# Kernel optimization log

Hardware: AMD Instinct MI355X
Metric: run time of the kernel (lower is better)

The kernel has to match this reference:

```python
import jax, jax.numpy as jnp
import numpy as np

B, TY, TX, TT, H, VS, VT = 32, 64, 64, 64, 512, 32000, 32000


def setup_inputs() -> dict:
    key = jax.random.key(0)
    ks = jax.random.split(key, 12)
    s = 0.05  # weight scale for numerical sanity
    return {
        "y_hidden": jax.random.normal(ks[0], (B, TY, H), jnp.float32),
        "y_hidden_null": jax.random.normal(ks[1], (1, H), jnp.float32),
        "target_state": jax.random.normal(ks[2], (B, TT, H), jnp.float32),
        "W_em": jax.random.normal(ks[3], (H, H), jnp.float32) * s,
        "b_em": jnp.zeros((H,), jnp.float32),
        "W_sv": jax.random.normal(ks[4], (H, VS), jnp.float32) * s,
        "b_sv": jnp.zeros((VS,), jnp.float32),
        "W_tv": jax.random.normal(ks[5], (H, VT), jnp.float32) * s,
        "b_tv": jnp.zeros((VT,), jnp.float32),
        "sources": jax.random.randint(ks[6], (B, TX), 0, VS, jnp.int32),
        "targets": jax.random.randint(ks[7], (B, TT), 0, VT, jnp.int32),
        "target_lengths": jax.random.randint(ks[8], (B,), 1, TT + 1, jnp.int32),
    }


def reference(y_hidden, y_hidden_null, target_state, W_em, b_em, W_sv, b_sv,
              W_tv, b_tv, sources, targets, target_lengths):
    # ---- emission (get_emission) ----
    ts = jnp.tanh(y_hidden @ W_em + b_em)            # (B, Ty, H)
    tsn = jnp.tanh(y_hidden_null @ W_em + b_em)      # (1, H)
    em_sm = jax.nn.softmax(ts @ W_sv + b_sv, axis=-1)        # (B, Ty, Vs)
    null_sm = jax.nn.softmax(tsn @ W_sv + b_sv, axis=-1)     # (1, Vs)
    # vectorized replacement of tf.map_fn + tf.gather: per-batch gather of source token columns
    em_g = jnp.take_along_axis(em_sm, sources[:, None, :], axis=-1)  # (B, Ty, Tx)
    null_g = null_sm[0][sources]                                     # (B, Tx)
    null_tiled = jnp.broadcast_to(null_g[:, None, :], (sources.shape[0], ts.shape[1], sources.shape[1]))
    emission_prob = jnp.concatenate([em_g, null_tiled], axis=1)      # (B, 2*Ty, Tx)

    # ---- reconstruction (get_target); keep_prob = 1 so dropout is identity ----
    tgt_sm = jax.nn.softmax(target_state @ W_tv + b_tv, axis=-1)     # (B, Tt, Vt)
    target_predicted = jnp.argmax(tgt_sm, axis=-1)                   # (B, Tt)
    # gather[t, targets[t]] then * eye then reduce_sum == diagonal pick: prob of own token
    target_prob = jnp.take_along_axis(tgt_sm, targets[:, :, None].astype(jnp.int32), axis=-1)[..., 0]  # (B, Tt)
    Tt = targets.shape[1]
    target_mask = (jnp.arange(Tt)[None, :] < target_lengths[:, None]).astype(target_prob.dtype)
    reconstruction_expectation = target_prob * target_mask
    reconstruction_expectation_log = jnp.log(target_prob) * target_mask
    return emission_prob, reconstruction_expectation, reconstruction_expectation_log, target_predicted
```

## Files before the change

### kernel.cpp

```cpp
#include <hip/hip_runtime.h>
#include <math.h>

#define H 512
#define V 32000
#define NVB 250

typedef unsigned short ushort_t;
typedef __attribute__((ext_vector_type(8))) short short8;
typedef __attribute__((ext_vector_type(4))) float f32x4;

__device__ __forceinline__ unsigned short f2bf(float x) {
    unsigned int u; __builtin_memcpy(&u, &x, 4);
    unsigned int r = (u + 0x7fffu + ((u >> 16) & 1u)) >> 16;
    return (unsigned short)r;
}
__device__ __forceinline__ float bfu2f(unsigned short h) {
    unsigned int u = ((unsigned int)h) << 16;
    float f; __builtin_memcpy(&f, &u, 4);
    return f;
}

__device__ __forceinline__ void t2_insert(float& m1, int& c1, float& m2, int& c2,
                                          float v, int idx) {
    if (v > m1 || (v == m1 && idx < c1)) { m2 = m1; c2 = c1; m1 = v; c1 = idx; }
    else if (v > m2 || (v == m2 && idx < c2)) { m2 = v; c2 = idx; }
}

__global__ __launch_bounds__(256) void k_emstate(
    const float* __restrict__ y_hidden, const float* __restrict__ y_null,
    const float* __restrict__ W, const float* __restrict__ bias,
    float* __restrict__ ts)
{
    const int NR = 2049;
    __shared__ float As[16][64];
    __shared__ float Bs[16][64];
    int rb = blockIdx.y, cb = blockIdx.x;
    int row0 = rb * 64, col0 = cb * 64;
    int tid = threadIdx.x;
    int tr = tid >> 4, tc = tid & 15;
    float acc[4][4] = {};
    for (int k0 = 0; k0 < H; k0 += 16) {
        {
            int r = tid >> 2;
            int kk = (tid & 3) << 2;
            int row = row0 + r;
            float4 v = make_float4(0.f, 0.f, 0.f, 0.f);
            if (row < 2048)       v = *(const float4*)&y_hidden[row * H + k0 + kk];
            else if (row == 2048) v = *(const float4*)&y_null[k0 + kk];
            As[kk + 0][r] = v.x; As[kk + 1][r] = v.y;
            As[kk + 2][r] = v.z; As[kk + 3][r] = v.w;
            int bk = tid >> 4, bc = (tid & 15) << 2;
            *(float4*)&Bs[bk][bc] = *(const float4*)&W[(k0 + bk) * H + col0 + bc];
        }
        __syncthreads();
#pragma unroll
        for (int kk = 0; kk < 16; ++kk) {
            float4 a = *(float4*)&As[kk][tr * 4];
            float4 b = *(float4*)&Bs[kk][tc * 4];
            float av[4] = {a.x, a.y, a.z, a.w};
            float bv[4] = {b.x, b.y, b.z, b.w};
#pragma unroll
            for (int i = 0; i < 4; i++)
#pragma unroll
                for (int j = 0; j < 4; j++) acc[i][j] += av[i] * bv[j];
        }
        __syncthreads();
    }
#pragma unroll
    for (int i = 0; i < 4; i++) {
        int row = row0 + tr * 4 + i;
        if (row >= NR) break;
#pragma unroll
        for (int j = 0; j < 4; j++) {
            int col = col0 + tc * 4 + j;
            ts[(size_t)row * H + col] = tanhf(acc[i][j] + bias[col]);
        }
    }
}

__global__ __launch_bounds__(256) void k_packA(
    const float* __restrict__ A, int nvalid, int nb16,
    ushort_t* __restrict__ Ph, ushort_t* __restrict__ Pl)
{
    int c = blockIdx.x * 256 + threadIdx.x;
    if (c >= nb16 * 1024) return;
    int n16 = c >> 10, rem = c & 1023, k32 = rem >> 6, l = rem & 63;
    int m = n16 * 16 + (l & 15);
    int k = k32 * 32 + (l >> 4) * 8;
    float v[8];
    if (m < nvalid) {
        *(float4*)&v[0] = *(const float4*)&A[(size_t)m * H + k];
        *(float4*)&v[4] = *(const float4*)&A[(size_t)m * H + k + 4];
    } else {
#pragma unroll
        for (int j = 0; j < 8; ++j) v[j] = 0.f;
    }
    unsigned int hh[4], lo[4];
#pragma unroll
    for (int p = 0; p < 4; ++p) {
        unsigned short h0 = f2bf(v[2 * p]), h1 = f2bf(v[2 * p + 1]);
        hh[p] = (unsigned int)h0 | ((unsigned int)h1 << 16);
        unsigned short l0 = f2bf(v[2 * p] - bfu2f(h0));
        unsigned short l1 = f2bf(v[2 * p + 1] - bfu2f(h1));
        lo[p] = (unsigned int)l0 | ((unsigned int)l1 << 16);
    }
    size_t o = ((size_t)n16 * 16 + k32) * 512 + l * 8;
    *(uint4*)&Ph[o] = make_uint4(hh[0], hh[1], hh[2], hh[3]);
    *(uint4*)&Pl[o] = make_uint4(lo[0], lo[1], lo[2], lo[3]);
}

__global__ __launch_bounds__(256) void k_packW(
    const float* __restrict__ W,
    ushort_t* __restrict__ Ph, ushort_t* __restrict__ Pl)
{
    int c = blockIdx.x * 256 + threadIdx.x;
    int n16 = c >> 10, rem = c & 1023, k32 = rem >> 6, l = rem & 63;
    int n = n16 * 16 + (l & 15);
    int k = k32 * 32 + (l >> 4) * 8;
    float v[8];
#pragma unroll
    for (int j = 0; j < 8; ++j) v[j] = W[(size_t)(k + j) * V + n];
    unsigned int hh[4], lo[4];
#pragma unroll
    for (int p = 0; p < 4; ++p) {
        unsigned short h0 = f2bf(v[2 * p]), h1 = f2bf(v[2 * p + 1]);
        hh[p] = (unsigned int)h0 | ((unsigned int)h1 << 16);
        unsigned short l0 = f2bf(v[2 * p] - bfu2f(h0));
        unsigned short l1 = f2bf(v[2 * p + 1] - bfu2f(h1));
        lo[p] = (unsigned int)l0 | ((unsigned int)l1 << 16);
    }
    size_t o = ((size_t)n16 * 16 + k32) * 512 + l * 8;
    *(uint4*)&Ph[o] = make_uint4(hh[0], hh[1], hh[2], hh[3]);
    *(uint4*)&Pl[o] = make_uint4(lo[0], lo[1], lo[2], lo[3]);
}

template<bool TOP2>
__global__ __launch_bounds__(256, 2) void k_gemm(
    int nrb,
    const ushort_t* __restrict__ Ah, const ushort_t* __restrict__ Al,
    const ushort_t* __restrict__ Bh, const ushort_t* __restrict__ Bl,
    const float* __restrict__ bias,
    float* __restrict__ pL,
    float* __restrict__ pM1, float* __restrict__ pM2,
    int* __restrict__ pI1, int* __restrict__ pI2)
{
    const int id  = blockIdx.x;
    const int xcd = id & 7;
    const int seq = id >> 3;
    const int rbg = xcd >> 2;
    const int vbg = xcd & 3;
    const int g0  = (nrb + 1) >> 1;
    const int nrbg = rbg ? (nrb - g0) : g0;
    const int vbl = seq / nrbg;
    const int rbl = seq - vbl * nrbg;
    const int vbsz = (vbg < 2) ? 63 : 62;
    if (vbl >= vbsz) return;
    const int rb = rbg ? (g0 + rbl) : rbl;
    const int vb = vbg * 63 - ((vbg == 3) ? 1 : 0) + vbl;

    __shared__ float sc_s[128][2];
    __shared__ float sc_m1[128][2], sc_m2[128][2];
    __shared__ int   sc_c1[128][2], sc_c2[128][2];

    const int tid = threadIdx.x;
    const int row0 = rb * 128, col0 = vb * 128;
    const int lane = tid & 63, w = tid >> 6;
    const int wy = w >> 1, wx = w & 1;

    f32x4 acc[4][4];
#pragma unroll
    for (int i = 0; i < 4; ++i)
#pragma unroll
        for (int j = 0; j < 4; ++j)
#pragma unroll
            for (int r = 0; r < 4; ++r) acc[i][j][r] = 0.f;

    int a_off[4], b_off[4];
#pragma unroll
    for (int i = 0; i < 4; ++i) {
        a_off[i] = ((rb * 8 + wy * 4 + i) * 16) * 512 + lane * 8;
        b_off[i] = ((vb * 8 + wx * 4 + i) * 16) * 512 + lane * 8;
    }

    short8 ah_[2][4], al_[2][4], bh_[2][4], bl_[2][4];

#define LOADC(S, IT) {                                                   \
    const int ko = (IT) * 512;                                           \
    _Pragma("unroll")                                                    \
    for (int i = 0; i < 4; ++i) {                                        \
        ah_[S][i] = *(const short8*)&Ah[a_off[i] + ko];                  \
        al_[S][i] = *(const short8*)&Al[a_off[i] + ko];                  \
        bh_[S][i] = *(const short8*)&Bh[b_off[i] + ko];                  \
        bl_[S][i] = *(const short8*)&Bl[b_off[i] + ko];                  \
    } }

#define MFMAS(S) {                                                       \
    _Pragma("unroll")                                                    \
    for (int i = 0; i < 4; ++i)                                          \
        _Pragma("unroll")                                                \
        for (int j = 0; j < 4; ++j) {                                    \
            acc[i][j] = __builtin_amdgcn_mfma_f32_16x16x32_bf16(         \
                ah_[S][i], bh_[S][j], acc[i][j], 0, 0, 0);               \
            acc[i][j] = __builtin_amdgcn_mfma_f32_16x16x32_bf16(         \
                ah_[S][i], bl_[S][j], acc[i][j], 0, 0, 0);               \
            acc[i][j] = __builtin_amdgcn_mfma_f32_16x16x32_bf16(         \
                al_[S][i], bh_[S][j], acc[i][j], 0, 0, 0);               \
        } }

    LOADC(0, 0)
#pragma unroll 1
    for (int it = 0; it < 16; it += 2) {
        LOADC(1, it + 1)
        MFMAS(0)
        if (it + 2 < 16) LOADC(0, it + 2)
        MFMAS(1)
    }
#undef LOADC
#undef MFMAS

    float b4[4];
#pragma unroll
    for (int j = 0; j < 4; ++j) b4[j] = bias[col0 + wx * 64 + j * 16 + (lane & 15)];
    const int colbase = col0 + wx * 64 + (lane & 15);

#pragma unroll
    for (int i = 0; i < 4; ++i) {
#pragma unroll
        for (int r = 0; r < 4; ++r) {
            float s = 0.f;
            float m1 = -3e38f, m2 = -3e38f; int c1 = 0x7fffffff, c2 = 0x7fffffff;
#pragma unroll
            for (int j = 0; j < 4; ++j) {
                float v = acc[i][j][r] + b4[j];
                s += __expf(v);
                if (TOP2) t2_insert(m1, c1, m2, c2, v, colbase + j * 16);
            }
            for (int st = 1; st < 16; st <<= 1) {
                s += __shfl_xor(s, st, 64);
                if (TOP2) {
                    float om1 = __shfl_xor(m1, st, 64); int oc1 = __shfl_xor(c1, st, 64);
                    float om2 = __shfl_xor(m2, st, 64); int oc2 = __shfl_xor(c2, st, 64);
                    t2_insert(m1, c1, m2, c2, om1, oc1);
                    t2_insert(m1, c1, m2, c2, om2, oc2);
                }
            }
            if ((lane & 15) == 0) {
                int rowLoc = wy * 64 + i * 16 + (lane >> 4) * 4 + r;
                sc_s[rowLoc][wx] = s;
                if (TOP2) {
                    sc_m1[rowLoc][wx] = m1; sc_c1[rowLoc][wx] = c1;
                    sc_m2[rowLoc][wx] = m2; sc_c2[rowLoc][wx] = c2;
                }
            }
        }
    }
    __syncthreads();
    if (tid < 128) {
        int rowG = row0 + tid;
        pL[(size_t)rowG * NVB + vb] = sc_s[tid][0] + sc_s[tid][1];
        if (TOP2) {
            float m1 = sc_m1[tid][0]; int c1 = sc_c1[tid][0];
            float m2 = sc_m2[tid][0]; int c2 = sc_c2[tid][0];
            t2_insert(m1, c1, m2, c2, sc_m1[tid][1], sc_c1[tid][1]);
            t2_insert(m1, c1, m2, c2, sc_m2[tid][1], sc_c2[tid][1]);
            pM1[(size_t)rowG * NVB + vb] = m1;
            pM2[(size_t)rowG * NVB + vb] = m2;
            pI1[(size_t)rowG * NVB + vb] = c1;
            pI2[(size_t)rowG * NVB + vb] = c2;
        }
    }
}

__global__ __launch_bounds__(256) void k_combine_src(
    const float* __restrict__ pL, int nrows, float* __restrict__ L)
{
    int w = threadIdx.x >> 6, ll = threadIdx.x & 63;
    int row = blockIdx.x * 4 + w;
    if (row >= nrows) return;
    const float* p = &pL[(size_t)row * NVB];
    float s = 0.f;
    for (int vb = ll; vb < NVB; vb += 64) s += p[vb];
    for (int st = 1; st < 64; st <<= 1) s += __shfl_xor(s, st, 64);
    if (ll == 0) L[row] = s;
}

__global__ __launch_bounds__(256) void k_combine_tgt(
    const float* __restrict__ pL,
    const float* __restrict__ pM1, const float* __restrict__ pM2,
    const int* __restrict__ pI1, const int* __restrict__ pI2,
    float* __restrict__ L, int* __restrict__ C0, int* __restrict__ C1)
{
    int w = threadIdx.x >> 6, ll = threadIdx.x & 63;
    int row = blockIdx.x * 4 + w;
    if (row >= 2048) return;
    size_t base = (size_t)row * NVB;
    float s = 0.f;
    float m1 = -3e38f, m2 = -3e38f; int c1 = 0x7fffffff, c2 = 0x7fffffff;
    for (int vb = ll; vb < NVB; vb += 64) {
        s += pL[base + vb];
        t2_insert(m1, c1, m2, c2, pM1[base + vb], pI1[base + vb]);
        t2_insert(m1, c1, m2, c2, pM2[base + vb], pI2[base + vb]);
    }
    for (int st = 1; st < 64; st <<= 1) {
        s += __shfl_xor(s, st, 64);
        float om1 = __shfl_xor(m1, st, 64); int oc1 = __shfl_xor(c1, st, 64);
        float om2 = __shfl_xor(m2, st, 64); int oc2 = __shfl_xor(c2, st, 64);
        t2_insert(m1, c1, m2, c2, om1, oc1);
        t2_insert(m1, c1, m2, c2, om2, oc2);
    }
    if (ll == 0) { L[row] = s; C0[row] = c1; C1[row] = c2; }
}

__global__ __launch_bounds__(256) void k_emission(
    const float* __restrict__ ts, const float* __restrict__ W_sv,
    const float* __restrict__ b_sv, const int* __restrict__ sources,
    const float* __restrict__ L, float* __restrict__ out)
{
    __shared__ float wcol[H];
    __shared__ float sbias;
    int b = blockIdx.y, tx = blockIdx.x;
    int tid = threadIdx.x;
    int s = sources[b * 64 + tx];
    wcol[tid]       = W_sv[(size_t)tid * V + s];
    wcol[tid + 256] = W_sv[(size_t)(tid + 256) * V + s];
    if (tid == 0) sbias = b_sv[s];
    __syncthreads();
    int w = tid >> 6, ll = tid & 63;
    for (int r = w; r <= 64; r += 4) {
        int row = (r < 64) ? (b * 64 + r) : 2048;
        const float* a = &ts[(size_t)row * H];
        float sum = 0.f;
#pragma unroll
        for (int j = 0; j < 8; ++j) sum += a[ll * 8 + j] * wcol[ll * 8 + j];
        for (int m2 = 1; m2 < 64; m2 <<= 1) sum += __shfl_xor(sum, m2, 64);
        float prob = __expf(sum + sbias) / L[row];
        if (r < 64) {
            if (ll == 0) out[b * 8192 + r * 64 + tx] = prob;
        } else {
            out[b * 8192 + (64 + ll) * 64 + tx] = prob;
        }
    }
}

__global__ __launch_bounds__(256) void k_target_final(
    const float* __restrict__ tstate,
    const float* __restrict__ W_tv, const float* __restrict__ b_tv,
    const int* __restrict__ targets, const int* __restrict__ tlen,
    const float* __restrict__ L, const int* __restrict__ C0,
    const int* __restrict__ C1,
    float* __restrict__ out_exp, float* __restrict__ out_log,
    float* __restrict__ out_pred)
{
    int w = threadIdx.x >> 6, ll = threadIdx.x & 63;
    int row = blockIdx.x * 4 + w;
    if (row >= 2048) return;
    int tok = targets[row], a0 = C0[row], a1 = C1[row];
    const float* a = &tstate[(size_t)row * H];
    float s0 = 0.f, s1 = 0.f, s2 = 0.f;
#pragma unroll
    for (int j = 0; j < 8; ++j) {
        int k = ll * 8 + j;
        float av = a[k];
        const float* wr = &W_tv[(size_t)k * V];
        s0 += av * wr[tok]; s1 += av * wr[a0]; s2 += av * wr[a1];
    }
    for (int st = 1; st < 64; st <<= 1) {
        s0 += __shfl_xor(s0, st, 64);
        s1 += __shfl_xor(s1, st, 64);
        s2 += __shfl_xor(s2, st, 64);
    }
    if (ll == 0) {
        float ltok = s0 + b_tv[tok];
        float v0 = s1 + b_tv[a0], v1 = s2 + b_tv[a1];
        int pred = (v1 > v0 || (v1 == v0 && a1 < a0)) ? a1 : a0;
        float Li = L[row];
        int bb = row >> 6, t = row & 63;
        int mask = (t < tlen[bb]) ? 1 : 0;
        float prob = __expf(ltok) / Li;
        out_exp[row]  = mask ? prob : 0.f;
        out_log[row]  = mask ? (ltok - __logf(Li)) : 0.f;
        out_pred[row] = (float)pred;
    }
}

extern "C" void kernel_launch(void* const* d_in, const int* in_sizes, int n_in,
                              void* d_out, int out_size, void* d_ws, size_t ws_size,
                              hipStream_t stream)
{
    const float* y_hidden = (const float*)d_in[0];
    const float* y_null   = (const float*)d_in[1];
    const float* tstate   = (const float*)d_in[2];
    const float* W_em     = (const float*)d_in[3];
    const float* b_em     = (const float*)d_in[4];
    const float* W_sv     = (const float*)d_in[5];
    const float* b_sv     = (const float*)d_in[6];
    const float* W_tv     = (const float*)d_in[7];
    const float* b_tv     = (const float*)d_in[8];
    const int*   sources  = (const int*)d_in[9];
    const int*   targets  = (const int*)d_in[10];
    const int*   tlen     = (const int*)d_in[11];

    float* out = (float*)d_out;
    float* out_em   = out;
    float* out_exp  = out + 262144;
    float* out_log  = out + 264192;
    float* out_pred = out + 266240;

    float* ws = (float*)d_ws;
    size_t off = 0;
    float*    ts    = ws + off; off += (size_t)2176 * H;
    ushort_t* tsPh  = (ushort_t*)(ws + off); off += (size_t)2176 * H / 2;
    ushort_t* tsPl  = (ushort_t*)(ws + off); off += (size_t)2176 * H / 2;
    ushort_t* ttPh  = (ushort_t*)(ws + off); off += (size_t)2048 * H / 2;
    ushort_t* ttPl  = (ushort_t*)(ws + off); off += (size_t)2048 * H / 2;
    ushort_t* Wh    = (ushort_t*)(ws + off); off += (size_t)V * H / 2;
    ushort_t* Wl    = (ushort_t*)(ws + off); off += (size_t)V * H / 2;
    float* pL0  = ws + off; off += (size_t)2176 * NVB;
    float* pL1  = ws + off; off += (size_t)2048 * NVB;
    float* pM1a = ws + off; off += (size_t)2048 * NVB;
    float* pM1b = ws + off; off += (size_t)2048 * NVB;
    int*   pI1a = (int*)(ws + off); off += (size_t)2048 * NVB;
    int*   pI1b = (int*)(ws + off); off += (size_t)2048 * NVB;
    float* L0   = ws + off; off += 2176;
    float* L1   = ws + off; off += 2048;
    int*   C0   = (int*)(ws + off); off += 2048;
    int*   C1   = (int*)(ws + off); off += 2048;

    k_emstate<<<dim3(8, 33), 256, 0, stream>>>(y_hidden, y_null, W_em, b_em, ts);

    k_packA<<<(136 * 1024) / 256, 256, 0, stream>>>(ts, 2049, 136, tsPh, tsPl);
    k_packA<<<(128 * 1024) / 256, 256, 0, stream>>>(tstate, 2048, 128, ttPh, ttPl);

    k_packW<<<(2000 * 1024) / 256, 256, 0, stream>>>(W_sv, Wh, Wl);
    k_gemm<false><<<dim3(8 * 567), 256, 0, stream>>>(
        17, tsPh, tsPl, Wh, Wl, b_sv, pL0, nullptr, nullptr, nullptr, nullptr);

    k_packW<<<(2000 * 1024) / 256, 256, 0, stream>>>(W_tv, Wh, Wl);
    k_gemm<true><<<dim3(8 * 504), 256, 0, stream>>>(
        16, ttPh, ttPl, Wh, Wl, b_tv, pL1, pM1a, pM1b, pI1a, pI1b);

    k_combine_src<<<(2049 + 3) / 4, 256, 0, stream>>>(pL0, 2049, L0);
    k_combine_tgt<<<2048 / 4, 256, 0, stream>>>(pL1, pM1a, pM1b, pI1a, pI1b,
                                                L1, C0, C1);

    k_emission<<<dim3(64, 32), 256, 0, stream>>>(ts, W_sv, b_sv, sources, L0, out_em);

    k_target_final<<<2048 / 4, 256, 0, stream>>>(tstate, W_tv, b_tv, targets, tlen,
                                                 L1, C0, C1,
                                                 out_exp, out_log, out_pred);
}
```

Before: 1.329 ms.

## Enlarge GEMM tiles to 256x256 with LDS staging via global_load_lds

The split-bf16 vocabulary GEMM now uses 256x256 output tiles computed by 512-thread blocks instead of 128x128 tiles with 256 threads. Operand fragments are no longer read from global memory straight into registers by each wave. They are staged into double-buffered LDS with direct global-to-LDS loads, and each chunk is shared across waves. Padding, workspace sizes and the partial softmax/top-2 write-out are adjusted to the new tiling. This cuts redundant global and L2 operand traffic. The cost is a large LDS footprint, likely one block per CU, and a barrier on every k-step.

```diff
diff --git a/kernel.cpp b/kernel.cpp
--- a/kernel.cpp
+++ b/kernel.cpp
@@ -24,6 +24,13 @@
                                           float v, int idx) {
     if (v > m1 || (v == m1 && idx < c1)) { m2 = m1; c2 = c1; m1 = v; c1 = idx; }
     else if (v > m2 || (v == m2 && idx < c2)) { m2 = v; c2 = idx; }
+}
+
+__device__ __forceinline__ void gl16(const void* g, void* l) {
+    __builtin_amdgcn_global_load_lds(
+        (const __attribute__((address_space(1))) void*)g,
+        (__attribute__((address_space(3))) void*)l,
+        16, 0, 0);
 }
 
 __global__ __launch_bounds__(256) void k_emstate(
@@ -135,7 +142,7 @@
 }
 
 template<bool TOP2>
-__global__ __launch_bounds__(256, 2) void k_gemm(
+__global__ __launch_bounds__(512, 2) void k_gemm(
     int nrb,
     const ushort_t* __restrict__ Ah, const ushort_t* __restrict__ Al,
     const ushort_t* __restrict__ Bh, const ushort_t* __restrict__ Bl,
@@ -153,78 +160,94 @@
     const int nrbg = rbg ? (nrb - g0) : g0;
     const int vbl = seq / nrbg;
     const int rbl = seq - vbl * nrbg;
-    const int vbsz = (vbg < 2) ? 63 : 62;
+    const int vbsz = (vbg == 0) ? 32 : 31;
     if (vbl >= vbsz) return;
     const int rb = rbg ? (g0 + rbl) : rbl;
-    const int vb = vbg * 63 - ((vbg == 3) ? 1 : 0) + vbl;
-
-    __shared__ float sc_s[128][2];
-    __shared__ float sc_m1[128][2], sc_m2[128][2];
-    __shared__ int   sc_c1[128][2], sc_c2[128][2];
+    const int vb = ((vbg == 0) ? 0 : (1 + 31 * vbg)) + vbl;
+
+    __shared__ __attribute__((aligned(16))) ushort_t AshB[2][16 * 512];
+    __shared__ __attribute__((aligned(16))) ushort_t AslB[2][16 * 512];
+    __shared__ __attribute__((aligned(16))) ushort_t BshB[2][16 * 512];
+    __shared__ __attribute__((aligned(16))) ushort_t BslB[2][16 * 512];
+    __shared__ float sc_s[256][4];
+    __shared__ float sc_m1[256][4], sc_m2[256][4];
+    __shared__ int   sc_c1[256][4], sc_c2[256][4];
 
     const int tid = threadIdx.x;
-    const int row0 = rb * 128, col0 = vb * 128;
     const int lane = tid & 63, w = tid >> 6;
-    const int wy = w >> 1, wx = w & 1;
-
-    f32x4 acc[4][4];
-#pragma unroll
-    for (int i = 0; i < 4; ++i)
+    const int wy = w >> 2, wx = w & 3;
+
+    f32x4 acc[8][4];
+#pragma unroll
+    for (int i = 0; i < 8; ++i)
 #pragma unroll
         for (int j = 0; j < 4; ++j)
 #pragma unroll
             for (int r = 0; r < 4; ++r) acc[i][j][r] = 0.f;
 
-    int a_off[4], b_off[4];
-#pragma unroll
-    for (int i = 0; i < 4; ++i) {
-        a_off[i] = ((rb * 8 + wy * 4 + i) * 16) * 512 + lane * 8;
-        b_off[i] = ((vb * 8 + wx * 4 + i) * 16) * 512 + lane * 8;
-    }
-
-    short8 ah_[2][4], al_[2][4], bh_[2][4], bl_[2][4];
-
-#define LOADC(S, IT) {                                                   \
-    const int ko = (IT) * 512;                                           \
+    const ushort_t* gsrc = (w < 2) ? Ah : (w < 4) ? Al : (w < 6) ? Bh : Bl;
+    ushort_t* base0 = (w < 2) ? AshB[0] : (w < 4) ? AslB[0] : (w < 6) ? BshB[0] : BslB[0];
+    ushort_t* base1 = (w < 2) ? AshB[1] : (w < 4) ? AslB[1] : (w < 6) ? BshB[1] : BslB[1];
+    const int half = (w & 1) * 8;
+    ushort_t* ldb0 = base0 + half * 512;
+    ushort_t* ldb1 = base1 + half * 512;
+    const size_t n16base = (size_t)(((w < 4) ? rb : vb) * 16 + half);
+
+#define STAGE(DST, IT)                                                   \
     _Pragma("unroll")                                                    \
-    for (int i = 0; i < 4; ++i) {                                        \
-        ah_[S][i] = *(const short8*)&Ah[a_off[i] + ko];                  \
-        al_[S][i] = *(const short8*)&Al[a_off[i] + ko];                  \
-        bh_[S][i] = *(const short8*)&Bh[b_off[i] + ko];                  \
-        bl_[S][i] = *(const short8*)&Bl[b_off[i] + ko];                  \
-    } }
-
-#define MFMAS(S) {                                                       \
+    for (int mb = 0; mb < 8; ++mb)                                       \
+        gl16(gsrc + (((n16base + mb) * 16 + (size_t)(IT)) << 9) + lane * 8, \
+             (DST) + mb * 512);
+
+#define STEP(BUF, IT, DOPREF)                                            \
+{                                                                        \
+    const ushort_t* cAh = AshB[BUF];                                     \
+    const ushort_t* cAl = AslB[BUF];                                     \
+    const ushort_t* cBh = BshB[BUF];                                     \
+    const ushort_t* cBl = BslB[BUF];                                     \
+    short8 bhf[4], blf[4];                                               \
     _Pragma("unroll")                                                    \
-    for (int i = 0; i < 4; ++i)                                          \
+    for (int j = 0; j < 4; ++j) {                                        \
+        bhf[j] = *(const short8*)&cBh[((wx * 4 + j) << 9) + (lane << 3)]; \
+        blf[j] = *(const short8*)&cBl[((wx * 4 + j) << 9) + (lane << 3)]; \
+    }                                                                    \
+    if (DOPREF) { STAGE((BUF) ? ldb0 : ldb1, (IT) + 1) }                 \
+    __builtin_amdgcn_sched_barrier(0);                                   \
+    _Pragma("unroll")                                                    \
+    for (int i = 0; i < 8; ++i) {                                        \
+        short8 ah = *(const short8*)&cAh[((wy * 8 + i) << 9) + (lane << 3)]; \
+        short8 al = *(const short8*)&cAl[((wy * 8 + i) << 9) + (lane << 3)]; \
         _Pragma("unroll")                                                \
         for (int j = 0; j < 4; ++j) {                                    \
-            acc[i][j] = __builtin_amdgcn_mfma_f32_16x16x32_bf16(         \
-                ah_[S][i], bh_[S][j], acc[i][j], 0, 0, 0);               \
-            acc[i][j] = __builtin_amdgcn_mfma_f32_16x16x32_bf16(         \
-                ah_[S][i], bl_[S][j], acc[i][j], 0, 0, 0);               \
-            acc[i][j] = __builtin_amdgcn_mfma_f32_16x16x32_bf16(         \
-                al_[S][i], bh_[S][j], acc[i][j], 0, 0, 0);               \
-        } }
-
-    LOADC(0, 0)
+            acc[i][j] = __builtin_amdgcn_mfma_f32_16x16x32_bf16(ah, bhf[j], acc[i][j], 0, 0, 0); \
+            acc[i][j] = __builtin_amdgcn_mfma_f32_16x16x32_bf16(ah, blf[j], acc[i][j], 0, 0, 0); \
+            acc[i][j] = __builtin_amdgcn_mfma_f32_16x16x32_bf16(al, bhf[j], acc[i][j], 0, 0, 0); \
+        }                                                                \
+    }                                                                    \
+    __builtin_amdgcn_sched_barrier(0);                                   \
+    __builtin_amdgcn_s_waitcnt(0x0F70);     \
+    __builtin_amdgcn_s_barrier();          \
+}
+
+    STAGE(ldb0, 0)
+    __builtin_amdgcn_s_waitcnt(0x0F70);
+    __builtin_amdgcn_s_barrier();
+
 #pragma unroll 1
     for (int it = 0; it < 16; it += 2) {
-        LOADC(1, it + 1)
-        MFMAS(0)
-        if (it + 2 < 16) LOADC(0, it + 2)
-        MFMAS(1)
-    }
-#undef LOADC
-#undef MFMAS
+        STEP(0, it, 1)
+        STEP(1, it + 1, (it + 2 < 16))
+    }
+#undef STAGE
+#undef STEP
 
     float b4[4];
 #pragma unroll
-    for (int j = 0; j < 4; ++j) b4[j] = bias[col0 + wx * 64 + j * 16 + (lane & 15)];
-    const int colbase = col0 + wx * 64 + (lane & 15);
-
-#pragma unroll
-    for (int i = 0; i < 4; ++i) {
+    for (int j = 0; j < 4; ++j) b4[j] = bias[vb * 256 + wx * 64 + j * 16 + (lane & 15)];
+    const int colbase = vb * 256 + wx * 64 + (lane & 15);
+
+#pragma unroll
+    for (int i = 0; i < 8; ++i) {
 #pragma unroll
         for (int r = 0; r < 4; ++r) {
             float s = 0.f;
@@ -245,7 +268,7 @@
                 }
             }
             if ((lane & 15) == 0) {
-                int rowLoc = wy * 64 + i * 16 + (lane >> 4) * 4 + r;
+                int rowLoc = wy * 128 + i * 16 + (lane >> 4) * 4 + r;
                 sc_s[rowLoc][wx] = s;
                 if (TOP2) {
                     sc_m1[rowLoc][wx] = m1; sc_c1[rowLoc][wx] = c1;
@@ -255,18 +278,23 @@
         }
     }
     __syncthreads();
-    if (tid < 128) {
-        int rowG = row0 + tid;
-        pL[(size_t)rowG * NVB + vb] = sc_s[tid][0] + sc_s[tid][1];
+    if (tid < 256) {
+        int rowG = rb * 256 + tid;
+        pL[(size_t)rowG * NVB + vb * 2 + 0] = sc_s[tid][0] + sc_s[tid][1];
+        pL[(size_t)rowG * NVB + vb * 2 + 1] = sc_s[tid][2] + sc_s[tid][3];
         if (TOP2) {
-            float m1 = sc_m1[tid][0]; int c1 = sc_c1[tid][0];
-            float m2 = sc_m2[tid][0]; int c2 = sc_c2[tid][0];
-            t2_insert(m1, c1, m2, c2, sc_m1[tid][1], sc_c1[tid][1]);
-            t2_insert(m1, c1, m2, c2, sc_m2[tid][1], sc_c2[tid][1]);
-            pM1[(size_t)rowG * NVB + vb] = m1;
-            pM2[(size_t)rowG * NVB + vb] = m2;
-            pI1[(size_t)rowG * NVB + vb] = c1;
-            pI2[(size_t)rowG * NVB + vb] = c2;
+#pragma unroll
+            for (int h = 0; h < 2; ++h) {
+                int g0i = h * 2, g1i = h * 2 + 1;
+                float m1 = sc_m1[tid][g0i]; int c1 = sc_c1[tid][g0i];
+                float m2 = sc_m2[tid][g0i]; int c2 = sc_c2[tid][g0i];
+                t2_insert(m1, c1, m2, c2, sc_m1[tid][g1i], sc_c1[tid][g1i]);
+                t2_insert(m1, c1, m2, c2, sc_m2[tid][g1i], sc_c2[tid][g1i]);
+                pM1[(size_t)rowG * NVB + vb * 2 + h] = m1;
+                pM2[(size_t)rowG * NVB + vb * 2 + h] = m2;
+                pI1[(size_t)rowG * NVB + vb * 2 + h] = c1;
+                pI2[(size_t)rowG * NVB + vb * 2 + h] = c2;
+            }
         }
     }
 }
@@ -409,13 +437,13 @@
     float* ws = (float*)d_ws;
     size_t off = 0;
     float*    ts    = ws + off; off += (size_t)2176 * H;
-    ushort_t* tsPh  = (ushort_t*)(ws + off); off += (size_t)2176 * H / 2;
-    ushort_t* tsPl  = (ushort_t*)(ws + off); off += (size_t)2176 * H / 2;
+    ushort_t* tsPh  = (ushort_t*)(ws + off); off += (size_t)2304 * H / 2;
+    ushort_t* tsPl  = (ushort_t*)(ws + off); off += (size_t)2304 * H / 2;
     ushort_t* ttPh  = (ushort_t*)(ws + off); off += (size_t)2048 * H / 2;
     ushort_t* ttPl  = (ushort_t*)(ws + off); off += (size_t)2048 * H / 2;
     ushort_t* Wh    = (ushort_t*)(ws + off); off += (size_t)V * H / 2;
     ushort_t* Wl    = (ushort_t*)(ws + off); off += (size_t)V * H / 2;
-    float* pL0  = ws + off; off += (size_t)2176 * NVB;
+    float* pL0  = ws + off; off += (size_t)2304 * NVB;
     float* pL1  = ws + off; off += (size_t)2048 * NVB;
     float* pM1a = ws + off; off += (size_t)2048 * NVB;
     float* pM1b = ws + off; off += (size_t)2048 * NVB;
@@ -428,16 +456,16 @@
 
     k_emstate<<<dim3(8, 33), 256, 0, stream>>>(y_hidden, y_null, W_em, b_em, ts);
 
-    k_packA<<<(136 * 1024) / 256, 256, 0, stream>>>(ts, 2049, 136, tsPh, tsPl);
+    k_packA<<<(144 * 1024) / 256, 256, 0, stream>>>(ts, 2049, 144, tsPh, tsPl);
     k_packA<<<(128 * 1024) / 256, 256, 0, stream>>>(tstate, 2048, 128, ttPh, ttPl);
 
     k_packW<<<(2000 * 1024) / 256, 256, 0, stream>>>(W_sv, Wh, Wl);
-    k_gemm<false><<<dim3(8 * 567), 256, 0, stream>>>(
-        17, tsPh, tsPl, Wh, Wl, b_sv, pL0, nullptr, nullptr, nullptr, nullptr);
+    k_gemm<false><<<dim3(8 * 160), 512, 0, stream>>>(
+        9, tsPh, tsPl, Wh, Wl, b_sv, pL0, nullptr, nullptr, nullptr, nullptr);
 
     k_packW<<<(2000 * 1024) / 256, 256, 0, stream>>>(W_tv, Wh, Wl);
-    k_gemm<true><<<dim3(8 * 504), 256, 0, stream>>>(
-        16, ttPh, ttPl, Wh, Wl, b_tv, pL1, pM1a, pM1b, pI1a, pI1b);
+    k_gemm<true><<<dim3(8 * 128), 512, 0, stream>>>(
+        8, ttPh, ttPl, Wh, Wl, b_tv, pL1, pM1a, pM1b, pI1a, pI1b);
 
     k_combine_src<<<(2049 + 3) / 4, 256, 0, stream>>>(pL0, 2049, L0);
     k_combine_tgt<<<2048 / 4, 256, 0, stream>>>(pL1, pM1a, pM1b, pI1a, pI1b,
```

Measured after the change: 1.310 ms. No clear change (-1.4%).
